# Performance work log

Measured on AMD Instinct MI355X. Metric: run time of the kernel, lower is better.

## Reference

```python
import jax, jax.numpy as jnp
import numpy as np

# Fixed multi-scale geometry implied by the module's hard-coded reshapes
# (48^2=2304, 24^2=576, 12^2=144; Len_q = 576).
SPATIAL = [(48, 48), (24, 24), (12, 12)]
NH, NP, NL = 6, 4, 3  # num_heads, num_points, num_levels


def _process_reference_points(rp):
    """rp: (B, 3024, 2) normalized refs over 3 levels -> (B, 576, 2).
    Mirrors the part1/part2/part3 averaging in MSDeformAttn.forward."""
    B = rp.shape[0]
    p1 = rp[:, :2304].reshape(B, 48, 48, 2).mean(axis=(1, 2))[:, None, :]
    p1 = jnp.broadcast_to(p1, (B, 576, 2))
    p2 = rp[:, 2304:2880].reshape(B, 576, 2)
    p3 = rp[:, 2880:].reshape(B, 12, 12, 2)
    p3 = jax.image.resize(p3, (B, 24, 24, 2), 'bilinear')  # align_corners=False
    p3 = p3.reshape(B, 576, 2)
    return (p1 + p2 + p3) / 3.0


def _bilinear_sample(val_l, coords, Hl, Wl):
    """val_l: (B, Hl*Wl, nh, d) one level's values.
    coords: (B, Lq, nh, P, 2) normalized (x, y) sampling locations.
    Returns (B, Lq, P, nh, d) bilinearly sampled values (zero padding)."""
    B, Lq, nh, P, _ = coords.shape
    px = coords[..., 0] * Wl - 0.5
    py = coords[..., 1] * Hl - 0.5
    x0 = jnp.floor(px)
    y0 = jnp.floor(py)
    lx = px - x0
    ly = py - y0
    x0i = x0.astype(jnp.int32)
    y0i = y0.astype(jnp.int32)

    def _flat(a):  # (B,Lq,nh,P) -> (B,Lq*P,nh,1) matching value layout
        return a.transpose(0, 1, 3, 2).reshape(B, Lq * P, nh, 1)

    def gather(xi, yi):
        valid = (xi >= 0) & (xi < Wl) & (yi >= 0) & (yi < Hl)
        xi_c = jnp.clip(xi, 0, Wl - 1)
        yi_c = jnp.clip(yi, 0, Hl - 1)
        idx = _flat(yi_c * Wl + xi_c)
        v = jnp.take_along_axis(val_l, idx, axis=1)  # (B,Lq*P,nh,d)
        return v * _flat(valid).astype(val_l.dtype)

    w00 = _flat((1 - lx) * (1 - ly))
    w10 = _flat(lx * (1 - ly))
    w01 = _flat((1 - lx) * ly)
    w11 = _flat(lx * ly)
    out = (gather(x0i, y0i) * w00 + gather(x0i + 1, y0i) * w10 +
           gather(x0i, y0i + 1) * w01 + gather(x0i + 1, y0i + 1) * w11)
    return out.reshape(B, Lq, P, nh, -1)


def setup_inputs() -> dict:
    key = jax.random.key(0)
    ks = jax.random.split(key, 8)
    B, C = 32, 384
    Lq, Lv = 576, 3024
    # reference points exactly as get_reference_points builds them
    refs = []
    for (Hl, Wl) in SPATIAL:
        ry, rx = np.meshgrid(np.linspace(0.5, Hl - 0.5, Hl) / Hl,
                             np.linspace(0.5, Wl - 0.5, Wl) / Wl, indexing='ij')
        refs.append(np.stack([rx.ravel(), ry.ravel()], -1))
    rp = np.concatenate(refs, 0).astype(np.float32)  # (3024, 2)
    rp = np.broadcast_to(rp[None, :, None, :], (B, Lv, 1, 2)).copy()
    s = 1.0 / np.sqrt(C)
    return {
        'query': jax.random.normal(ks[0], (B, Lq, C), jnp.float32),
        'value': jax.random.normal(ks[1], (B, Lv, C), jnp.float32),
        'reference_points': jnp.asarray(rp),
        'W_value': jax.random.normal(ks[2], (C, C), jnp.float32) * s,
        'b_value': jnp.zeros((C,), jnp.float32),
        'W_off': jax.random.normal(ks[3], (C, NH * NL * NP * 2), jnp.float32) * 0.01,
        'b_off': jnp.zeros((NH * NL * NP * 2,), jnp.float32),
        'W_attn': jax.random.normal(ks[4], (C, NH * NL * NP), jnp.float32) * s,
        'b_attn': jnp.zeros((NH * NL * NP,), jnp.float32),
        'W_out': jax.random.normal(ks[5], (C, C), jnp.float32) * s,
        'b_out': jnp.zeros((C,), jnp.float32),
    }


def reference(query, value, reference_points, W_value, b_value, W_off, b_off,
              W_attn, b_attn, W_out, b_out):
    B, Lq, C = query.shape
    d = C // NH
    val = (value @ W_value + b_value).reshape(B, -1, NH, d)
    off = (query @ W_off + b_off).reshape(B, Lq, NH, NL, NP, 2)
    attn = jax.nn.softmax((query @ W_attn + b_attn)
                          .reshape(B, Lq, NH, NL * NP), axis=-1)
    attn = attn.reshape(B, Lq, NH, NL, NP)
    ref = _process_reference_points(reference_points.reshape(B, -1, 2))
    coords = off + ref[:, :, None, None, None, :]  # (B,Lq,nh,L,P,2)
    out = jnp.zeros((B, Lq, NH, d), query.dtype)
    start = 0
    for l, (Hl, Wl) in enumerate(SPATIAL):
        val_l = val[:, start:start + Hl * Wl]
        sampled = _bilinear_sample(val_l, coords[:, :, :, l], Hl, Wl)
        out = out + jnp.einsum('bqpnd,bqnp->bqnd', sampled, attn[:, :, :, l])
        start += Hl * Wl
    return out.reshape(B, Lq, NH * d) @ W_out + b_out
```

## Files before the change

kernel.cpp:

```cpp
#include <hip/hip_runtime.h>
#include <cmath>

#define B_SZ   32
#define LQ     576
#define LV     3024
#define CDIM   384
#define NHEAD  6
#define DHEAD  64
#define NLVL   3
#define NPTS   4
#define NPROJ  216
#define NPROJP 256

typedef short    bx4 __attribute__((ext_vector_type(4)));
typedef short    bx8 __attribute__((ext_vector_type(8)));
typedef float    fx4 __attribute__((ext_vector_type(4)));
typedef _Float16 hx8 __attribute__((ext_vector_type(8)));

__device__ __forceinline__ short f2bf(float f) {
    unsigned u = __builtin_bit_cast(unsigned, f);
    unsigned r = (u + 0x7FFFu + ((u >> 16) & 1u)) >> 16;
    return (short)r;
}
__device__ __forceinline__ float bf2f(unsigned short u) {
    return __builtin_bit_cast(float, ((unsigned)u) << 16);
}
__device__ __forceinline__ short f2h(float f) {
    return __builtin_bit_cast(short, (_Float16)f);
}

__global__ __launch_bounds__(256) void cast_transpose_kernel(
    const float* __restrict__ W, short* __restrict__ Wt, int K, int N)
{
    int idx = blockIdx.x * 256 + threadIdx.x;
    if (idx >= K * N) return;
    int n = idx / K, k = idx - n * K;
    Wt[idx] = f2bf(W[(size_t)k * N + n]);
}

__global__ __launch_bounds__(256) void prep_proj_f16_kernel(
    const float* __restrict__ W_off, const float* __restrict__ b_off,
    const float* __restrict__ W_attn, const float* __restrict__ b_attn,
    short* __restrict__ Wf, float* __restrict__ bc)
{
    int idx = blockIdx.x * 256 + threadIdx.x;
    if (idx >= NPROJP * CDIM) return;
    int n = idx / CDIM, k = idx - n * CDIM;
    float w = 0.f;
    if (n < 144)           w = W_off[(size_t)k * 144 + n];
    else if (n < NPROJ)    w = W_attn[(size_t)k * 72 + (n - 144)];
    Wf[idx] = f2h(w);
    if (idx < NPROJP)
        bc[idx] = (idx < 144) ? b_off[idx]
                 : (idx < NPROJ ? b_attn[idx - 144] : 0.f);
}

__global__ __launch_bounds__(256) void value_gemm_kernel(
    const float* __restrict__ A, const short* __restrict__ Bt,
    const float* __restrict__ bias, short* __restrict__ Cout,
    int M, int K)
{
    constexpr int N = 384;
    __shared__ short As[64 * 64];
    __shared__ short Bs[192 * 64];

    const int tid = threadIdx.x;
    const int m0 = blockIdx.x * 64;
    const int n0 = blockIdx.y * 192;

    const int w  = tid >> 6;
    const int l  = tid & 63;
    const int wc = w * 48;
    const int lr = l & 15;
    const int q  = l >> 4;

    const int rg  = l >> 3;
    const int cg  = l & 7;
    const int csw = cg ^ rg;

    const int ar   = tid >> 4;
    const int kq   = (tid & 15) << 2;
    const int oct  = kq >> 3;
    const int koff = kq & 7;
    const int aswz = ((oct ^ (ar & 7)) << 3) + koff;
    const float* gA0 = A + (size_t)(m0 + ar) * K + kq;

    fx4 acc[4][3] = {};

    for (int k0 = 0; k0 < K; k0 += 64) {
        #pragma unroll
        for (int u = 0; u < 6; ++u) {
            const int rbase = w * 48 + u * 8;
            const short* gB = Bt + (size_t)(n0 + rbase + rg) * K + k0 + csw * 8;
            __builtin_amdgcn_global_load_lds(
                (const __attribute__((address_space(1))) void*)gB,
                (__attribute__((address_space(3))) void*)&Bs[rbase * 64],
                16, 0, 0);
        }
        #pragma unroll
        for (int p = 0; p < 4; ++p) {
            const int row = p * 16 + ar;
            const float4 v = *(const float4*)(gA0 + (size_t)p * 16 * K + k0);
            bx4 s;
            s[0] = f2bf(v.x); s[1] = f2bf(v.y); s[2] = f2bf(v.z); s[3] = f2bf(v.w);
            *(bx4*)&As[row * 64 + aswz] = s;
        }
        __syncthreads();

        #pragma unroll
        for (int ks = 0; ks < 2; ++ks) {
            bx8 af[4], bf[3];
            #pragma unroll
            for (int i = 0; i < 4; ++i)
                af[i] = *(const bx8*)&As[(i * 16 + lr) * 64 +
                                         (((ks * 4 + q) ^ (lr & 7)) << 3)];
            #pragma unroll
            for (int j = 0; j < 3; ++j)
                bf[j] = *(const bx8*)&Bs[(wc + j * 16 + lr) * 64 +
                                         (((ks * 4 + q) ^ (lr & 7)) << 3)];
            #pragma unroll
            for (int i = 0; i < 4; ++i)
                #pragma unroll
                for (int j = 0; j < 3; ++j)
                    acc[i][j] = __builtin_amdgcn_mfma_f32_16x16x32_bf16(
                        af[i], bf[j], acc[i][j], 0, 0, 0);
        }
        __syncthreads();
    }

    float bv[3];
    #pragma unroll
    for (int j = 0; j < 3; ++j) bv[j] = bias[n0 + wc + j * 16 + lr];
    const int rrow = q * 4;
    #pragma unroll
    for (int i = 0; i < 4; ++i) {
        #pragma unroll
        for (int r = 0; r < 4; ++r) {
            const int row = m0 + i * 16 + rrow + r;
            #pragma unroll
            for (int j = 0; j < 3; ++j) {
                const int col = n0 + wc + j * 16 + lr;
                Cout[(size_t)row * N + col] = f2bf(acc[i][j][r] + bv[j]);
            }
        }
    }
}

template <bool OUT_BF16>
__global__ __launch_bounds__(256) void gemm_dma_kernel(
    const short* __restrict__ A, const short* __restrict__ Bt,
    const float* __restrict__ bias, void* __restrict__ Cout,
    int M, int K)
{
    constexpr int N = 384;
    __shared__ short As[128 * 64];
    __shared__ short Bs[128 * 64];

    const int tid = threadIdx.x;
    const int n0 = blockIdx.x * 128;
    const int m0 = blockIdx.y * 128;

    const int w  = tid >> 6;
    const int l  = tid & 63;
    const int wr = (w & 1) * 64;
    const int wc = (w >> 1) * 64;
    const int lr = l & 15;
    const int q  = l >> 4;

    const int rg  = l >> 3;
    const int cg  = l & 7;
    const int csw = cg ^ rg;

    fx4 acc[4][4] = {};

    for (int k0 = 0; k0 < K; k0 += 64) {
        #pragma unroll
        for (int t = 0; t < 4; ++t) {
            const int rbase = w * 32 + t * 8;
            const short* gA = A + (size_t)(m0 + rbase + rg) * K + k0 + csw * 8;
            __builtin_amdgcn_global_load_lds(
                (const __attribute__((address_space(1))) void*)gA,
                (__attribute__((address_space(3))) void*)&As[rbase * 64],
                16, 0, 0);
            const short* gB = Bt + (size_t)(n0 + rbase + rg) * K + k0 + csw * 8;
            __builtin_amdgcn_global_load_lds(
                (const __attribute__((address_space(1))) void*)gB,
                (__attribute__((address_space(3))) void*)&Bs[rbase * 64],
                16, 0, 0);
        }
        __syncthreads();

        #pragma unroll
        for (int ks = 0; ks < 2; ++ks) {
            bx8 af[4], bf[4];
            #pragma unroll
            for (int i = 0; i < 4; ++i)
                af[i] = *(const bx8*)&As[(wr + i * 16 + lr) * 64 +
                                         (((ks * 4 + q) ^ (lr & 7)) << 3)];
            #pragma unroll
            for (int j = 0; j < 4; ++j)
                bf[j] = *(const bx8*)&Bs[(wc + j * 16 + lr) * 64 +
                                         (((ks * 4 + q) ^ (lr & 7)) << 3)];
            #pragma unroll
            for (int i = 0; i < 4; ++i)
                #pragma unroll
                for (int j = 0; j < 4; ++j)
                    acc[i][j] = __builtin_amdgcn_mfma_f32_16x16x32_bf16(
                        af[i], bf[j], acc[i][j], 0, 0, 0);
        }
        __syncthreads();
    }

    const int rrow = q * 4;
    #pragma unroll
    for (int j = 0; j < 4; ++j) {
        const int col = n0 + wc + j * 16 + lr;
        const float bv = bias[col];
        #pragma unroll
        for (int i = 0; i < 4; ++i) {
            const int row = m0 + wr + i * 16 + rrow;
            #pragma unroll
            for (int r = 0; r < 4; ++r) {
                if (OUT_BF16)
                    ((short*)Cout)[(size_t)(row + r) * N + col] = f2bf(acc[i][j][r] + bv);
                else
                    ((float*)Cout)[(size_t)(row + r) * N + col] = acc[i][j][r] + bv;
            }
        }
    }
}

__global__ __launch_bounds__(256) void gemm_proj_kernel(
    const float* __restrict__ A, const short* __restrict__ Wf,
    const float* __restrict__ bias, float* __restrict__ C,
    int M, int K)
{
    __shared__ short As[128 * 72];
    __shared__ short Bs[128 * 72];

    const int tid = threadIdx.x;
    const int n0 = blockIdx.x * 128;
    const int m0 = blockIdx.y * 128;

    const int w  = tid >> 6;
    const int l  = tid & 63;
    const int wr = (w & 1) * 64;
    const int wc = (w >> 1) * 64;
    const int lr = l & 15;
    const int ko = (l >> 4) * 8;

    fx4 acc[4][4] = {};

    for (int k0 = 0; k0 < K; k0 += 64) {
        #pragma unroll
        for (int r = 0; r < 8; ++r) {
            const int id = tid + r * 256;
            const int m  = id >> 4;
            const int kq = (id & 15) << 2;
            const float4 v = *(const float4*)(A + (size_t)(m0 + m) * K + k0 + kq);
            bx4 s;
            s[0] = f2h(v.x); s[1] = f2h(v.y); s[2] = f2h(v.z); s[3] = f2h(v.w);
            *(bx4*)&As[m * 72 + kq] = s;
        }
        #pragma unroll
        for (int r = 0; r < 4; ++r) {
            const int id = tid + r * 256;
            const int n  = id >> 3;
            const int k8 = (id & 7) << 3;
            *(bx8*)&Bs[n * 72 + k8] = *(const bx8*)(Wf + (size_t)(n0 + n) * K + k0 + k8);
        }
        __syncthreads();

        #pragma unroll
        for (int ks = 0; ks < 2; ++ks) {
            bx8 af[4], bf[4];
            #pragma unroll
            for (int i = 0; i < 4; ++i)
                af[i] = *(const bx8*)&As[(wr + i * 16 + lr) * 72 + ks * 32 + ko];
            #pragma unroll
            for (int j = 0; j < 4; ++j)
                bf[j] = *(const bx8*)&Bs[(wc + j * 16 + lr) * 72 + ks * 32 + ko];
            #pragma unroll
            for (int i = 0; i < 4; ++i)
                #pragma unroll
                for (int j = 0; j < 4; ++j)
                    acc[i][j] = __builtin_amdgcn_mfma_f32_16x16x32_f16(
                        __builtin_bit_cast(hx8, af[i]),
                        __builtin_bit_cast(hx8, bf[j]), acc[i][j], 0, 0, 0);
        }
        __syncthreads();
    }

    const int rrow = (l >> 4) * 4;
    #pragma unroll
    for (int j = 0; j < 4; ++j) {
        const int col = n0 + wc + j * 16 + lr;
        if (col >= NPROJ) continue;
        const float bv = bias[col];
        #pragma unroll
        for (int i = 0; i < 4; ++i) {
            const int row = m0 + wr + i * 16 + rrow;
            #pragma unroll
            for (int r = 0; r < 4; ++r)
                C[(size_t)(row + r) * NPROJ + col] = acc[i][j][r] + bv;
        }
    }
}

__global__ __launch_bounds__(256) void ref_kernel(
    const float* __restrict__ rp, float* __restrict__ refp)
{
    const int b = blockIdx.x;
    const float* r = rp + (size_t)b * LV * 2;
    const int tid = threadIdx.x;

    __shared__ float redx[256], redy[256];
    float sx = 0.f, sy = 0.f;
    for (int i = tid; i < 2304; i += 256) {
        sx += r[2 * i + 0];
        sy += r[2 * i + 1];
    }
    redx[tid] = sx; redy[tid] = sy;
    __syncthreads();
    for (int s = 128; s > 0; s >>= 1) {
        if (tid < s) { redx[tid] += redx[tid + s]; redy[tid] += redy[tid + s]; }
        __syncthreads();
    }
    const float p1x = redx[0] * (1.f / 2304.f);
    const float p1y = redy[0] * (1.f / 2304.f);

    const float* g = r + 2880 * 2;
    for (int q = tid; q < 576; q += 256) {
        const float p2x = r[(2304 + q) * 2 + 0];
        const float p2y = r[(2304 + q) * 2 + 1];
        const int qy = q / 24, qx = q % 24;
        const float syc = fminf(fmaxf(0.5f * qy - 0.25f, 0.f), 11.f);
        const float sxc = fminf(fmaxf(0.5f * qx - 0.25f, 0.f), 11.f);
        int y0 = min((int)syc, 10);
        int x0 = min((int)sxc, 10);
        const float fy = syc - (float)y0, fx = sxc - (float)x0;
        const float v00x = g[(y0 * 12 + x0) * 2 + 0],     v00y = g[(y0 * 12 + x0) * 2 + 1];
        const float v10x = g[(y0 * 12 + x0 + 1) * 2 + 0], v10y = g[(y0 * 12 + x0 + 1) * 2 + 1];
        const float v01x = g[((y0 + 1) * 12 + x0) * 2 + 0],     v01y = g[((y0 + 1) * 12 + x0) * 2 + 1];
        const float v11x = g[((y0 + 1) * 12 + x0 + 1) * 2 + 0], v11y = g[((y0 + 1) * 12 + x0 + 1) * 2 + 1];
        const float p3x = (1.f - fy) * ((1.f - fx) * v00x + fx * v10x)
                        + fy * ((1.f - fx) * v01x + fx * v11x);
        const float p3y = (1.f - fy) * ((1.f - fx) * v00y + fx * v10y)
                        + fy * ((1.f - fx) * v01y + fx * v11y);
        refp[((size_t)b * LQ + q) * 2 + 0] = (p1x + p2x + p3x) * (1.f / 3.f);
        refp[((size_t)b * LQ + q) * 2 + 1] = (p1y + p2y + p3y) * (1.f / 3.f);
    }
}

__global__ __launch_bounds__(192) void sample_kernel(
    const unsigned short* __restrict__ val, const float* __restrict__ proj,
    const float* __restrict__ refp, unsigned* __restrict__ mid)
{
    const int i = blockIdx.x;
    const int g = i & 7;
    const int r = i >> 3;
    const int b = g * 4 + (r / LQ);
    const int q = r - (r / LQ) * LQ;
    const int bq = b * LQ + q;
    const int tid = threadIdx.x;

    __shared__ float attn[72];
    __shared__ int   sloc[72][4];
    __shared__ float swt[72][4];

    if (tid < 72) {
        attn[tid] = proj[(size_t)bq * NPROJ + 144 + tid];

        const int h = tid / 12;
        const int rr = tid % 12;
        const int l = rr >> 2;
        const int p = rr & 3;

        const int HL[3] = {48, 24, 12};
        const int ST[3] = {0, 2304, 2880};
        const int Hl = HL[l], Wl = HL[l], st = ST[l];

        const float rx = refp[bq * 2 + 0];
        const float ry = refp[bq * 2 + 1];
        const int oc = ((h * NLVL + l) * NPTS + p) * 2;
        const float cx = proj[(size_t)bq * NPROJ + oc + 0] + rx;
        const float cy = proj[(size_t)bq * NPROJ + oc + 1] + ry;

        const float px = cx * (float)Wl - 0.5f;
        const float py = cy * (float)Hl - 0.5f;
        const float x0f = floorf(px), y0f = floorf(py);
        const float lx = px - x0f, ly = py - y0f;
        const int x0 = (int)x0f, y0 = (int)y0f;

        #pragma unroll
        for (int k = 0; k < 4; ++k) {
            const int dx = k & 1, dy = k >> 1;
            const int xi = x0 + dx, yi = y0 + dy;
            const bool v = (xi >= 0) && (xi < Wl) && (yi >= 0) && (yi < Hl);
            const int xc = min(max(xi, 0), Wl - 1);
            const int yc = min(max(yi, 0), Hl - 1);
            sloc[tid][k] = st + yc * Wl + xc;
            const float wx = dx ? lx : 1.f - lx;
            const float wy = dy ? ly : 1.f - ly;
            swt[tid][k] = v ? wx * wy : 0.f;
        }
    }
    __syncthreads();

    if (tid < NHEAD) {
        float mx = -1e30f;
        #pragma unroll
        for (int j = 0; j < 12; ++j) mx = fmaxf(mx, attn[tid * 12 + j]);
        float s = 0.f;
        #pragma unroll
        for (int j = 0; j < 12; ++j) {
            const float e = expf(attn[tid * 12 + j] - mx);
            attn[tid * 12 + j] = e;
            s += e;
        }
        const float inv = 1.f / s;
        #pragma unroll
        for (int j = 0; j < 12; ++j) attn[tid * 12 + j] *= inv;
    }
    __syncthreads();

    const int h  = tid >> 5;
    const int c2 = (tid & 31) << 1;
    const unsigned* vp = (const unsigned*)(val + (size_t)b * LV * CDIM + h * DHEAD + c2);
    float acc0 = 0.f, acc1 = 0.f;
    #pragma unroll
    for (int s = 0; s < 12; ++s) {
        const int j = h * 12 + s;
        const float a = attn[j];
        float s0 = 0.f, s1 = 0.f;
        #pragma unroll
        for (int k = 0; k < 4; ++k) {
            const unsigned u = vp[(size_t)sloc[j][k] * (CDIM / 2)];
            const float lo = __builtin_bit_cast(float, u << 16);
            const float hi = __builtin_bit_cast(float, u & 0xFFFF0000u);
            s0 += swt[j][k] * lo;
            s1 += swt[j][k] * hi;
        }
        acc0 += a * s0;
        acc1 += a * s1;
    }
    const unsigned lo = (unsigned)(unsigned short)f2bf(acc0);
    const unsigned hi = (unsigned)(unsigned short)f2bf(acc1);
    mid[((size_t)bq * CDIM + h * DHEAD + c2) >> 1] = lo | (hi << 16);
}

extern "C" void kernel_launch(void* const* d_in, const int* in_sizes, int n_in,
                              void* d_out, int out_size, void* d_ws, size_t ws_size,
                              hipStream_t stream)
{
    (void)in_sizes; (void)n_in; (void)out_size; (void)ws_size;

    const float* query   = (const float*)d_in[0];
    const float* value   = (const float*)d_in[1];
    const float* rp      = (const float*)d_in[2];
    const float* W_value = (const float*)d_in[3];
    const float* b_value = (const float*)d_in[4];
    const float* W_off   = (const float*)d_in[5];
    const float* b_off   = (const float*)d_in[6];
    const float* W_attn  = (const float*)d_in[7];
    const float* b_attn  = (const float*)d_in[8];
    const float* W_out   = (const float*)d_in[9];
    const float* b_out   = (const float*)d_in[10];
    float* out = (float*)d_out;

    char* p = (char*)d_ws;
    auto take = [&](size_t bytes) { char* q = p; p += (bytes + 255) & ~(size_t)255; return q; };
    short* val  = (short*)take((size_t)B_SZ * LV * CDIM * 2);
    short* mid  = (short*)take((size_t)B_SZ * LQ * CDIM * 2);
    short* Wtv  = (short*)take((size_t)CDIM * CDIM * 2);
    short* Wto  = (short*)take((size_t)CDIM * CDIM * 2);
    short* Wf   = (short*)take((size_t)NPROJP * CDIM * 2);
    float* proj = (float*)take((size_t)B_SZ * LQ * NPROJ * 4);
    float* refp = (float*)take((size_t)B_SZ * LQ * 2 * 4);
    float* bc   = (float*)take((size_t)NPROJP * 4);

    const int Mv = B_SZ * LV;
    const int Mq = B_SZ * LQ;

    cast_transpose_kernel<<<(CDIM * CDIM + 255) / 256, 256, 0, stream>>>(
        W_value, Wtv, CDIM, CDIM);
    cast_transpose_kernel<<<(CDIM * CDIM + 255) / 256, 256, 0, stream>>>(
        W_out, Wto, CDIM, CDIM);
    prep_proj_f16_kernel<<<(NPROJP * CDIM + 255) / 256, 256, 0, stream>>>(
        W_off, b_off, W_attn, b_attn, Wf, bc);

    value_gemm_kernel<<<dim3(Mv / 64, 2), 256, 0, stream>>>(
        value, Wtv, b_value, val, Mv, CDIM);
    gemm_proj_kernel<<<dim3(2, Mq / 128), 256, 0, stream>>>(
        query, Wf, bc, proj, Mq, CDIM);
    ref_kernel<<<B_SZ, 256, 0, stream>>>(rp, refp);
    sample_kernel<<<Mq, 192, 0, stream>>>(
        (const unsigned short*)val, proj, refp, (unsigned*)mid);
    gemm_dma_kernel<false><<<dim3(3, Mq / 128), 256, 0, stream>>>(
        mid, Wto, b_out, out, Mq, CDIM);
}
```

Before: 388.0 us.

## Double-buffer value GEMM shared-memory tiles to overlap loads with MFMA

Converts the value-projection GEMM main loop into a two-stage pipeline. Shared memory for the A and B tiles is doubled, and the next K-tile's global loads (A into registers, B via direct global-to-LDS) are issued before the current tile's MFMAs. A is converted and written after compute, so one barrier per iteration replaces two and load latency can hide behind compute. The loop is hard-coded to 6 iterations (K=384), and the larger LDS footprint and extra live registers may lower occupancy.

```diff
diff --git a/kernel.cpp b/kernel.cpp
--- a/kernel.cpp
+++ b/kernel.cpp
@@ -61,8 +61,8 @@
     int M, int K)
 {
     constexpr int N = 384;
-    __shared__ short As[64 * 64];
-    __shared__ short Bs[192 * 64];
+    __shared__ short As[2][64 * 64];
+    __shared__ short Bs[2][192 * 64];
 
     const int tid = threadIdx.x;
     const int m0 = blockIdx.x * 64;
@@ -86,38 +86,60 @@
     const float* gA0 = A + (size_t)(m0 + ar) * K + kq;
 
     fx4 acc[4][3] = {};
-
-    for (int k0 = 0; k0 < K; k0 += 64) {
+    float4 v0, v1, v2, v3;
+
+    auto issueB = [&](int buf, int t) {
         #pragma unroll
         for (int u = 0; u < 6; ++u) {
             const int rbase = w * 48 + u * 8;
-            const short* gB = Bt + (size_t)(n0 + rbase + rg) * K + k0 + csw * 8;
+            const short* gB = Bt + (size_t)(n0 + rbase + rg) * K + t * 64 + csw * 8;
             __builtin_amdgcn_global_load_lds(
                 (const __attribute__((address_space(1))) void*)gB,
-                (__attribute__((address_space(3))) void*)&Bs[rbase * 64],
+                (__attribute__((address_space(3))) void*)&Bs[buf][rbase * 64],
                 16, 0, 0);
         }
-        #pragma unroll
-        for (int p = 0; p < 4; ++p) {
-            const int row = p * 16 + ar;
-            const float4 v = *(const float4*)(gA0 + (size_t)p * 16 * K + k0);
-            bx4 s;
-            s[0] = f2bf(v.x); s[1] = f2bf(v.y); s[2] = f2bf(v.z); s[3] = f2bf(v.w);
-            *(bx4*)&As[row * 64 + aswz] = s;
-        }
-        __syncthreads();
+    };
+    auto loadA = [&](int t) {
+        const float* g = gA0 + t * 64;
+        v0 = *(const float4*)(g);
+        v1 = *(const float4*)(g + (size_t)16 * K);
+        v2 = *(const float4*)(g + (size_t)32 * K);
+        v3 = *(const float4*)(g + (size_t)48 * K);
+    };
+    auto writeA = [&](int buf) {
+        bx4 s;
+        s[0]=f2bf(v0.x); s[1]=f2bf(v0.y); s[2]=f2bf(v0.z); s[3]=f2bf(v0.w);
+        *(bx4*)&As[buf][(ar +  0) * 64 + aswz] = s;
+        s[0]=f2bf(v1.x); s[1]=f2bf(v1.y); s[2]=f2bf(v1.z); s[3]=f2bf(v1.w);
+        *(bx4*)&As[buf][(ar + 16) * 64 + aswz] = s;
+        s[0]=f2bf(v2.x); s[1]=f2bf(v2.y); s[2]=f2bf(v2.z); s[3]=f2bf(v2.w);
+        *(bx4*)&As[buf][(ar + 32) * 64 + aswz] = s;
+        s[0]=f2bf(v3.x); s[1]=f2bf(v3.y); s[2]=f2bf(v3.z); s[3]=f2bf(v3.w);
+        *(bx4*)&As[buf][(ar + 48) * 64 + aswz] = s;
+    };
+
+    issueB(0, 0);
+    loadA(0);
+    writeA(0);
+    __syncthreads();
+
+    #pragma unroll
+    for (int t = 0; t < 6; ++t) {
+        const int cur = t & 1;
+
+        if (t < 5) { loadA(t + 1); issueB(cur ^ 1, t + 1); }
 
         #pragma unroll
         for (int ks = 0; ks < 2; ++ks) {
             bx8 af[4], bf[3];
             #pragma unroll
             for (int i = 0; i < 4; ++i)
-                af[i] = *(const bx8*)&As[(i * 16 + lr) * 64 +
-                                         (((ks * 4 + q) ^ (lr & 7)) << 3)];
+                af[i] = *(const bx8*)&As[cur][(i * 16 + lr) * 64 +
+                                             (((ks * 4 + q) ^ (lr & 7)) << 3)];
             #pragma unroll
             for (int j = 0; j < 3; ++j)
-                bf[j] = *(const bx8*)&Bs[(wc + j * 16 + lr) * 64 +
-                                         (((ks * 4 + q) ^ (lr & 7)) << 3)];
+                bf[j] = *(const bx8*)&Bs[cur][(wc + j * 16 + lr) * 64 +
+                                             (((ks * 4 + q) ^ (lr & 7)) << 3)];
             #pragma unroll
             for (int i = 0; i < 4; ++i)
                 #pragma unroll
@@ -125,6 +147,9 @@
                     acc[i][j] = __builtin_amdgcn_mfma_f32_16x16x32_bf16(
                         af[i], bf[j], acc[i][j], 0, 0, 0);
         }
+
+        if (t < 5) writeA(cur ^ 1);
+
         __syncthreads();
     }
 
```

After: 391.7 us. Within noise of the previous version (+1.0%).
